# Kernel tuning notes

Hardware: AMD Instinct MI355X
Metric: run time of the kernel (lower is better)

The kernel has to match this reference:

```python
import jax, jax.numpy as jnp
import numpy as np

B, NW, LW = 128, 64, 32
TD, PD = 108, 19
F = PD + TD + 1   # feat_dim = 128
M = 128           # model_dim


def _linear_params(key, din, dout):
    kw, _ = jax.random.split(key)
    W = jax.random.normal(kw, (din, dout), jnp.float32) * 0.02
    b = jnp.zeros((dout,), jnp.float32)
    return W, b


def setup_inputs() -> dict:
    key = jax.random.key(0)
    ks = jax.random.split(key, 12)
    time_features = jax.random.normal(ks[0], (B, NW, LW, TD), jnp.float32)
    position_pos_features = jax.random.normal(ks[1], (B, NW, LW, PD), jnp.float32)
    position_neg_features = jax.random.normal(ks[2], (B, NW, LW, PD), jnp.float32)
    weight = jax.random.uniform(ks[3], (B, NW, LW), jnp.float32)
    # sign in {-1, +1} (0 would zero the step; walks are signed edges)
    sign = (2 * jax.random.randint(ks[4], (B, NW, LW), 0, 2) - 1).astype(jnp.int32)
    Wq, bq = _linear_params(ks[5], F, F)
    Wk, bk = _linear_params(ks[6], F, F)
    Wv, bv = _linear_params(ks[7], F, F)
    Wl, bl = _linear_params(ks[8], F, M)
    Wqp, bqp = _linear_params(ks[9], M, M)
    Wkp, bkp = _linear_params(ks[10], M, M)
    Wvp, bvp = _linear_params(ks[11], M, M)
    return dict(time_features=time_features,
                position_pos_features=position_pos_features,
                position_neg_features=position_neg_features,
                weight=weight, sign=sign,
                Wq=Wq, bq=bq, Wk=Wk, bk=bk, Wv=Wv, bv=bv,
                Wl=Wl, bl=bl,
                Wqp=Wqp, bqp=bqp, Wkp=Wkp, bkp=bkp, Wvp=Wvp, bvp=bvp)


def _self_attn_sum(x, Wq, bq, Wk, bk, Wv, bv):
    # x: [..., L, D]; manual scaled-dot attention, scale = sqrt(input_size)
    d = x.shape[-1]
    q = x @ Wq + bq
    k = x @ Wk + bk
    v = x @ Wv + bv
    scores = jnp.einsum('...ld,...md->...lm', q, k) / jnp.sqrt(jnp.float32(d))
    w = jax.nn.softmax(scores, axis=-1)
    av = jnp.einsum('...lm,...md->...ld', w, v)
    return av.sum(axis=-2)  # sum over query positions


def reference(time_features, position_pos_features, position_neg_features,
              weight, sign,
              Wq, bq, Wk, bk, Wv, bv, Wl, bl,
              Wqp, bqp, Wkp, bkp, Wvp, bvp):
    # concat_features (note arg swap in forward_one_node): [pos_feat, time_feat, weight]
    cp = jnp.concatenate([position_pos_features, time_features, weight[..., None]], axis=-1)
    cn = jnp.concatenate([position_neg_features, time_features, weight[..., None]], axis=-1)
    pm = (sign > 0)[..., None]
    nm = (sign < 0)[..., None]
    zero = jnp.zeros((), cp.dtype)
    positive = jnp.where(pm, cp, zero) + jnp.where(nm, cn, zero)  # [B,NW,LW,F]
    negative = jnp.where(pm, cn, zero) + jnp.where(nm, cp, zero)
    # per-walk self-attention over len_walk, summed -> [B,NW,F]
    pos_emb = _self_attn_sum(positive, Wq, bq, Wk, bk, Wv, bv)
    neg_emb = _self_attn_sum(negative, Wq, bq, Wk, bk, Wv, bv)
    # set_node_embedding_act linear (no nonlinearity in source)
    pos_emb = pos_emb @ Wl + bl  # [B,NW,M]
    neg_emb = neg_emb @ Wl + bl
    # path attention over n_walk, summed -> [B,M]
    pos = _self_attn_sum(pos_emb, Wqp, bqp, Wkp, bkp, Wvp, bvp)
    neg = _self_attn_sum(neg_emb, Wqp, bqp, Wkp, bkp, Wvp, bvp)
    return (pos, neg)
```

## Files before the change

### kernel.cpp

```cpp
#include <hip/hip_runtime.h>
#include <hip/hip_bf16.h>

typedef __hip_bfloat16 bf16;
typedef unsigned short u16;
typedef unsigned int   u32;
typedef __attribute__((ext_vector_type(8))) short short8;
typedef __attribute__((ext_vector_type(4))) float f32x4;
typedef __attribute__((ext_vector_type(4))) unsigned int u32x4;

#define SCALE 0.08838834764831845f
#define MFMA  __builtin_amdgcn_mfma_f32_16x16x32_bf16

__device__ __forceinline__ float u2f(u16 x) { return __uint_as_float(((u32)x) << 16); }
__device__ __forceinline__ u16   f2u(float f) {
    __hip_bfloat16 h = __float2bfloat16(f);
    return *reinterpret_cast<u16*>(&h);
}
__device__ __forceinline__ float lo16(u32 w){ return __uint_as_float(w << 16); }
__device__ __forceinline__ float hi16(u32 w){ return __uint_as_float(w & 0xffff0000u); }
__device__ __forceinline__ int swz(int row, int col){ return (row << 7) | (col ^ ((row & 7) << 3)); }

__global__ void prep_aq(const float* __restrict__ Wq,  const float* __restrict__ Wk,
                        const float* __restrict__ bq,
                        const float* __restrict__ Wqp, const float* __restrict__ Wkp,
                        const float* __restrict__ bqp,
                        u16* __restrict__ frag, float* __restrict__ vv) {
    const int b = blockIdx.x;
    const int p = b / 33, sub = b % 33;
    const float* WA = p ? Wqp : Wq;
    const float* WB = p ? Wkp : Wk;
    const float* bA = p ? bqp : bq;
    if (sub < 32) {
        const int nt = sub >> 2, kc = sub & 3;
        u16* dst = frag + p * 16384 + sub * 512;
        for (int e = threadIdx.x; e < 512; e += 256) {
            const int lane = e >> 3, j = e & 7;
            const int k = kc * 32 + ((lane >> 4) << 3) + j;
            const int n = nt * 16 + (lane & 15);
            float a = 0.f;
            for (int cc = 0; cc < 128; cc += 4) {
                const float4 wa = *(const float4*)(WA + k * 128 + cc);
                const float4 wb = *(const float4*)(WB + n * 128 + cc);
                a += wa.x * wb.x + wa.y * wb.y + wa.z * wb.z + wa.w * wb.w;
            }
            dst[e] = f2u(a * SCALE);
        }
    } else {
        for (int d = threadIdx.x; d < 128; d += 256) {
            float a = 0.f;
            for (int cc = 0; cc < 128; cc++) a += WB[d * 128 + cc] * bA[cc];
            vv[p * 128 + d] = a;
        }
    }
}

__global__ void prep_wvl(const float* __restrict__ Wv, const float* __restrict__ bv,
                         const float* __restrict__ Wl, const float* __restrict__ bl,
                         u16* __restrict__ wvlT, float* __restrict__ bvl) {
    const int d = threadIdx.x;
    const int e = blockIdx.x;
    if (e < 128) {
        float a = 0.f;
        for (int cc = 0; cc < 128; cc++) a += Wv[e * 128 + cc] * Wl[cc * 128 + d];
        wvlT[(d >> 1) * 256 + e * 2 + (d & 1)] = f2u(a);
    } else {
        float a = bl[d];
        for (int cc = 0; cc < 128; cc++) a += 32.f * bv[cc] * Wl[cc * 128 + d];
        bvl[d] = a;
    }
}

__global__ __launch_bounds__(256) void rwa_walk_wave(
    const float* __restrict__ timef, const float* __restrict__ ppf,
    const float* __restrict__ pnf,  const float* __restrict__ wgt,
    const int*  __restrict__ sgn,
    const u16* __restrict__ fragQ,
    const float* __restrict__ vk,
    const u16* __restrict__ wvlT,
    const float* __restrict__ bvl,
    u16* __restrict__ emb)
{
    __shared__ __align__(16) u16 XS[4][4096];
    const int t  = threadIdx.x;
    const int wv = t >> 6, l = t & 63;
    const int wid  = blockIdx.x * 4 + wv;
    const int walk = wid >> 1, side = wid & 1;
    const int c = l & 15, g = l >> 4;
    u16* const xw = &XS[wv][0];

    const int row = l & 31, h = l >> 5;
    const int tok = walk * 32 + row;
    const float* tfp = timef + tok * 108;
    const float* pb = ((sgn[tok] > 0) == (side == 0)) ? (ppf + tok * 19) : (pnf + tok * 19);
    float ra = 0.f;
    #pragma unroll
    for (int ch = 0; ch < 8; ch++) {
        float tmp[8];
        #pragma unroll
        for (int j = 0; j < 8; j++) {
            const int hf = ch * 8 + j;
            float val;
            if (h == 0) {
                val = (hf < 19) ? pb[hf] : tfp[hf - 19];
            } else {
                val = (hf < 63) ? tfp[45 + hf] : wgt[tok];
            }
            tmp[j] = val;
        }
        const float4 k4a = *(const float4*)(vk + h * 64 + ch * 8);
        const float4 k4b = *(const float4*)(vk + h * 64 + ch * 8 + 4);
        ra += tmp[0] * k4a.x + tmp[1] * k4a.y + tmp[2] * k4a.z + tmp[3] * k4a.w
            + tmp[4] * k4b.x + tmp[5] * k4b.y + tmp[6] * k4b.z + tmp[7] * k4b.w;
        short8 pk;
        #pragma unroll
        for (int j = 0; j < 8; j++) pk[j] = (short)f2u(tmp[j]);
        *(short8*)&xw[swz(row, h * 64 + ch * 8)] = pk;
    }
    ra += __shfl_xor(ra, 32);
    ra *= SCALE;

    short8 af[2][4];
    #pragma unroll
    for (int it = 0; it < 2; it++)
        #pragma unroll
        for (int kc = 0; kc < 4; kc++)
            af[it][kc] = *(const short8*)&xw[swz(it * 16 + c, kc * 32 + g * 8)];

    #pragma unroll
    for (int nt = 0; nt < 8; nt++) {
        f32x4 a0 = {0.f, 0.f, 0.f, 0.f}, a1 = {0.f, 0.f, 0.f, 0.f};
        #pragma unroll
        for (int kc = 0; kc < 4; kc++) {
            const short8 bf = *(const short8*)(fragQ + ((nt * 4 + kc) * 64 + l) * 8);
            a0 = MFMA(af[0][kc], bf, a0, 0, 0, 0);
            a1 = MFMA(af[1][kc], bf, a1, 0, 0, 0);
        }
        #pragma unroll
        for (int r = 0; r < 4; r++) {
            xw[swz(g * 4 + r,      nt * 16 + c)] = f2u(a0[r]);
            xw[swz(16 + g * 4 + r, nt * 16 + c)] = f2u(a1[r]);
        }
    }

    f32x4 sa[2][2];
    #pragma unroll
    for (int it = 0; it < 2; it++) {
        short8 tg[4];
        #pragma unroll
        for (int kc = 0; kc < 4; kc++)
            tg[kc] = *(const short8*)&xw[swz(it * 16 + c, kc * 32 + g * 8)];
        #pragma unroll
        for (int jt = 0; jt < 2; jt++) {
            f32x4 acc = {0.f, 0.f, 0.f, 0.f};
            #pragma unroll
            for (int kc = 0; kc < 4; kc++)
                acc = MFMA(tg[kc], af[jt][kc], acc, 0, 0, 0);
            sa[it][jt] = acc;
        }
    }
    const float ra0 = __shfl(ra, c);
    const float ra1 = __shfl(ra, 16 + c);
    float cs0 = 0.f, cs1 = 0.f;
    #pragma unroll
    for (int it = 0; it < 2; it++)
    #pragma unroll
    for (int r = 0; r < 4; r++) {
        const float s0v = sa[it][0][r] + ra0;
        const float s1v = sa[it][1][r] + ra1;
        float m0 = fmaxf(s0v, s1v);
        m0 = fmaxf(m0, __shfl_xor(m0, 1));
        m0 = fmaxf(m0, __shfl_xor(m0, 2));
        m0 = fmaxf(m0, __shfl_xor(m0, 4));
        m0 = fmaxf(m0, __shfl_xor(m0, 8));
        const float p0 = __expf(s0v - m0);
        const float p1 = __expf(s1v - m0);
        float sm = p0 + p1;
        sm += __shfl_xor(sm, 1); sm += __shfl_xor(sm, 2);
        sm += __shfl_xor(sm, 4); sm += __shfl_xor(sm, 8);
        const float inv = 1.f / sm;
        cs0 += p0 * inv; cs1 += p1 * inv;
    }
    cs0 += __shfl_xor(cs0, 16); cs0 += __shfl_xor(cs0, 32);
    cs1 += __shfl_xor(cs1, 16); cs1 += __shfl_xor(cs1, 32);

    #pragma unroll
    for (int it = 0; it < 2; it++)
        #pragma unroll
        for (int kc = 0; kc < 4; kc++)
            *(short8*)&xw[swz(it * 16 + c, kc * 32 + g * 8)] = af[it][kc];

    float y0 = 0.f, y1v = 0.f;
    #pragma unroll
    for (int j = 0; j < 16; j++) {
        const float cj = __shfl(cs0, j);
        const u32 xv = *(const u32*)&xw[swz(j, 2 * l)];
        y0 += cj * lo16(xv); y1v += cj * hi16(xv);
    }
    #pragma unroll
    for (int j = 0; j < 16; j++) {
        const float cj = __shfl(cs1, j);
        const u32 xv = *(const u32*)&xw[swz(16 + j, 2 * l)];
        y0 += cj * lo16(xv); y1v += cj * hi16(xv);
    }

    float* const yb = (float*)xw;
    *(float2*)&yb[2 * l] = make_float2(y0, y1v);

    const float2 bb = *(const float2*)&bvl[2 * l];
    float e0 = bb.x, e1 = bb.y;
    const u32* wrow = (const u32*)wvlT + l * 128;
    const float4* yf = (const float4*)yb;
    #pragma unroll
    for (int eq = 0; eq < 32; eq++) {
        const u32x4 w4 = *(const u32x4*)(wrow + 4 * eq);
        const float4 y4 = yf[eq];
        e0 += y4.x * lo16(w4[0]) + y4.y * lo16(w4[1]) + y4.z * lo16(w4[2]) + y4.w * lo16(w4[3]);
        e1 += y4.x * hi16(w4[0]) + y4.y * hi16(w4[1]) + y4.z * hi16(w4[2]) + y4.w * hi16(w4[3]);
    }
    const u32 pk = (u32)f2u(e0) | ((u32)f2u(e1) << 16);
    ((u32*)emb)[(side * 8192 + walk) * 64 + l] = pk;
}

__global__ __launch_bounds__(256) void rwa_path_wave(
    const u16* __restrict__ embg, const u16* __restrict__ fragP,
    const float* __restrict__ vp, const float* __restrict__ Wvp,
    const float* __restrict__ bvp, float* __restrict__ out)
{
    __shared__ __align__(16) u16 ES[8192];
    __shared__ __align__(16) u16 TS[8192];
    __shared__ float raS[64];
    __shared__ float csP[4][64];
    __shared__ float y2S[4][128];
    __shared__ float y2F[128];
    __shared__ float outS[4][128];
    const int t  = threadIdx.x;
    const int sb = blockIdx.x;
    const int wv = t >> 6, l = t & 63;
    const int c = l & 15, g = l >> 4;

    {
        const int row = t >> 2, q = t & 3;
        const u16* src = embg + (size_t)sb * 8192 + row * 128 + q * 32;
        const float* vq = vp + q * 32;
        float p = 0.f;
        #pragma unroll
        for (int i = 0; i < 4; i++) {
            const short8 ev = *(const short8*)(src + 8 * i);
            #pragma unroll
            for (int j = 0; j < 8; j++) p += u2f((u16)ev[j]) * vq[8 * i + j];
            *(short8*)&ES[swz(row, q * 32 + 8 * i)] = ev;
        }
        p += __shfl_xor(p, 1);
        p += __shfl_xor(p, 2);
        if (q == 0) raS[row] = p * SCALE;
    }
    __syncthreads();

    {
        const int it = wv;
        short8 afr[4];
        #pragma unroll
        for (int kc = 0; kc < 4; kc++)
            afr[kc] = *(const short8*)&ES[swz(it * 16 + c, kc * 32 + g * 8)];
        #pragma unroll
        for (int nt = 0; nt < 8; nt++) {
            f32x4 acc = {0.f, 0.f, 0.f, 0.f};
            #pragma unroll
            for (int kc = 0; kc < 4; kc++) {
                const short8 bf = *(const short8*)(fragP + ((nt * 4 + kc) * 64 + l) * 8);
                acc = MFMA(afr[kc], bf, acc, 0, 0, 0);
            }
            #pragma unroll
            for (int r = 0; r < 4; r++)
                TS[swz(it * 16 + g * 4 + r, nt * 16 + c)] = f2u(acc[r]);
        }
    }
    __syncthreads();

    {
        const int it = wv;
        short8 tg[4];
        #pragma unroll
        for (int kc = 0; kc < 4; kc++)
            tg[kc] = *(const short8*)&TS[swz(it * 16 + c, kc * 32 + g * 8)];
        f32x4 sa[4];
        float raj[4];
        #pragma unroll
        for (int jt = 0; jt < 4; jt++) {
            f32x4 acc = {0.f, 0.f, 0.f, 0.f};
            #pragma unroll
            for (int kc = 0; kc < 4; kc++) {
                const short8 be = *(const short8*)&ES[swz(jt * 16 + c, kc * 32 + g * 8)];
                acc = MFMA(tg[kc], be, acc, 0, 0, 0);
            }
            sa[jt] = acc;
            raj[jt] = raS[jt * 16 + c];
        }
        float cs[4] = {0.f, 0.f, 0.f, 0.f};
        #pragma unroll
        for (int r = 0; r < 4; r++) {
            float p0 = sa[0][r] + raj[0], p1 = sa[1][r] + raj[1];
            float p2 = sa[2][r] + raj[2], p3 = sa[3][r] + raj[3];
            float m0 = fmaxf(fmaxf(p0, p1), fmaxf(p2, p3));
            m0 = fmaxf(m0, __shfl_xor(m0, 1));
            m0 = fmaxf(m0, __shfl_xor(m0, 2));
            m0 = fmaxf(m0, __shfl_xor(m0, 4));
            m0 = fmaxf(m0, __shfl_xor(m0, 8));
            p0 = __expf(p0 - m0); p1 = __expf(p1 - m0);
            p2 = __expf(p2 - m0); p3 = __expf(p3 - m0);
            float sm = p0 + p1 + p2 + p3;
            sm += __shfl_xor(sm, 1); sm += __shfl_xor(sm, 2);
            sm += __shfl_xor(sm, 4); sm += __shfl_xor(sm, 8);
            const float inv = 1.f / sm;
            cs[0] += p0 * inv; cs[1] += p1 * inv; cs[2] += p2 * inv; cs[3] += p3 * inv;
        }
        #pragma unroll
        for (int jt = 0; jt < 4; jt++) {
            cs[jt] += __shfl_xor(cs[jt], 16);
            cs[jt] += __shfl_xor(cs[jt], 32);
        }
        if (g == 0) {
            #pragma unroll
            for (int jt = 0; jt < 4; jt++) csP[wv][jt * 16 + c] = cs[jt];
        }
    }
    __syncthreads();

    {
        float y0 = 0.f, y1v = 0.f;
        #pragma unroll
        for (int jj = 0; jj < 16; jj++) {
            const int j = wv * 16 + jj;
            const float cj = csP[0][j] + csP[1][j] + csP[2][j] + csP[3][j];
            const u32 xv = *(const u32*)&ES[swz(j, 2 * l)];
            y0 += cj * lo16(xv); y1v += cj * hi16(xv);
        }
        y2S[wv][2 * l] = y0; y2S[wv][2 * l + 1] = y1v;
    }
    __syncthreads();
    if (t < 128) y2F[t] = y2S[0][t] + y2S[1][t] + y2S[2][t] + y2S[3][t];
    __syncthreads();

    {
        float o0 = 0.f, o1 = 0.f;
        const float2* w2p = (const float2*)Wvp;
        #pragma unroll
        for (int k = 0; k < 32; k++) {
            const int e = wv * 32 + k;
            const float ye = y2F[e];
            const float2 w2 = w2p[e * 64 + l];
            o0 += ye * w2.x; o1 += ye * w2.y;
        }
        outS[wv][2 * l] = o0; outS[wv][2 * l + 1] = o1;
    }
    __syncthreads();
    if (t < 128)
        out[sb * 128 + t] = 64.f * bvp[t] + outS[0][t] + outS[1][t] + outS[2][t] + outS[3][t];
}

__global__ __launch_bounds__(256) void rwa_fused_fb(
    const float* timef, const float* ppf, const float* pnf, const float* wgt,
    const int* __restrict__ sgn,
    const float* Wq, const float* bq, const float* Wk, const float* bk,
    const float* Wv, const float* bv, const float* Wl, const float* bl,
    const float* Wqp, const float* bqp, const float* Wkp, const float* bkp,
    const float* Wvp, const float* bvp, float* out)
{
    extern __shared__ __align__(16) char S[];
    char* const U = S;
    float (* const sc)[33]     = (float(*)[33])(S + 41088);
    u16   (* const embs)[128]  = (u16  (*)[128])(S + 45312);
    float* const csumA         = (float*)(S + 61696);
    float* const y1            = (float*)(S + 61824);
    float* const e1            = (float*)(S + 62336);
    u16   (* const xs)[128]   = (u16  (*)[128])U;
    float (* const qs)[128]   = (float(*)[128])(U + 8192);
    float (* const ks)[129]   = (float(*)[129])(U + 8192 + 16384);
    float (* const k2s)[129]  = (float(*)[129])U;
    float (* const qrow)[128] = (float(*)[128])(U + 33024);
    float (* const csum2)[64] = (float(*)[64])(U + 35072);

    const int t    = threadIdx.x;
    const int side = blockIdx.x >> 7;
    const int b    = blockIdx.x & 127;
    const int wv_  = t >> 6;
    const int lane = t & 63;

    for (int w = 0; w < 64; ++w) {
        const int tokb = (b * 64 + w) * 32;
        for (int o = t; o < 32 * 128; o += 256) {
            const int l = o >> 7, f = o & 127;
            const int tok = tokb + l;
            float v;
            if (f < 19) {
                const bool takeP = (sgn[tok] > 0) == (side == 0);
                v = takeP ? ppf[tok * 19 + f] : pnf[tok * 19 + f];
            } else if (f < 127) v = timef[tok * 108 + (f - 19)];
            else v = wgt[tok];
            xs[l][f] = f2u(v);
        }
        __syncthreads();
        {
            const int d = t & 127, l0 = t >> 7;
            float aq[16], ak[16];
            const float bqv = bq[d], bkv = bk[d];
            #pragma unroll
            for (int i = 0; i < 16; i++) { aq[i] = bqv; ak[i] = bkv; }
            for (int e = 0; e < 128; e += 4) {
                float xv[16][4];
                #pragma unroll
                for (int i = 0; i < 16; i++) {
                    const ushort4 u = *(const ushort4*)&xs[l0 + 2 * i][e];
                    xv[i][0] = u2f(u.x); xv[i][1] = u2f(u.y);
                    xv[i][2] = u2f(u.z); xv[i][3] = u2f(u.w);
                }
                #pragma unroll
                for (int r = 0; r < 4; r++) {
                    const float wq = Wq[(e + r) * 128 + d];
                    const float wk = Wk[(e + r) * 128 + d];
                    #pragma unroll
                    for (int i = 0; i < 16; i++) {
                        aq[i] += xv[i][r] * wq; ak[i] += xv[i][r] * wk;
                    }
                }
            }
            #pragma unroll
            for (int i = 0; i < 16; i++) { const int l = l0 + 2 * i; qs[l][d] = aq[i]; ks[l][d] = ak[i]; }
        }
        __syncthreads();
        for (int o = t; o < 1024; o += 256) {
            const int i = o >> 5, j = o & 31;
            float a0 = 0, a1 = 0, a2 = 0, a3 = 0;
            for (int e = 0; e < 128; e += 4) {
                const float4 q4 = *(const float4*)&qs[i][e];
                a0 += q4.x * ks[j][e];     a1 += q4.y * ks[j][e + 1];
                a2 += q4.z * ks[j][e + 2]; a3 += q4.w * ks[j][e + 3];
            }
            sc[i][j] = (a0 + a1 + a2 + a3) * SCALE;
        }
        __syncthreads();
        if (t < 32) {
            float m = -1e30f;
            for (int j = 0; j < 32; j++) m = fmaxf(m, sc[t][j]);
            float s = 0.f;
            for (int j = 0; j < 32; j++) { const float e0 = __expf(sc[t][j] - m); sc[t][j] = e0; s += e0; }
            const float inv = 1.f / s;
            for (int j = 0; j < 32; j++) sc[t][j] *= inv;
        }
        __syncthreads();
        if (t < 32) { float s = 0.f; for (int i = 0; i < 32; i++) s += sc[i][t]; csumA[t] = s; }
        __syncthreads();
        if (t < 128) { float a = 0.f; for (int j = 0; j < 32; j++) a += csumA[j] * u2f(xs[j][t]); y1[t] = a; }
        __syncthreads();
        if (t < 128) {
            float a = 32.f * bv[t];
            for (int e = 0; e < 128; e++) a += y1[e] * Wv[e * 128 + t];
            e1[t] = a;
        }
        __syncthreads();
        if (t < 128) {
            float a = bl[t];
            for (int f = 0; f < 128; f++) a += e1[f] * Wl[f * 128 + t];
            embs[w][t] = f2u(a);
        }
        __syncthreads();
    }
    {
        const int d = t & 127, j0 = t >> 7;
        float ak2[32];
        const float bkv = bkp[d];
        #pragma unroll
        for (int i = 0; i < 32; i++) ak2[i] = bkv;
        for (int e = 0; e < 128; e++) {
            const float wk = Wkp[e * 128 + d];
            #pragma unroll
            for (int i = 0; i < 32; i++) ak2[i] += u2f(embs[j0 + 2 * i][e]) * wk;
        }
        #pragma unroll
        for (int i = 0; i < 32; i++) k2s[j0 + 2 * i][d] = ak2[i];
    }
    csum2[wv_][lane] = 0.f;
    __syncthreads();
    for (int i0 = 0; i0 < 64; i0 += 4) {
        const int r = i0 + wv_;
        {
            float a0 = bqp[lane], a1 = bqp[lane + 64];
            for (int e = 0; e < 128; e++) {
                const float xv = u2f(embs[r][e]);
                a0 += xv * Wqp[e * 128 + lane];
                a1 += xv * Wqp[e * 128 + lane + 64];
            }
            qrow[wv_][lane] = a0; qrow[wv_][lane + 64] = a1;
        }
        {
            const int j = lane;
            float s = 0.f;
            for (int e = 0; e < 128; e += 4) {
                const float4 q4 = *(const float4*)&qrow[wv_][e];
                s += q4.x * k2s[j][e] + q4.y * k2s[j][e + 1] + q4.z * k2s[j][e + 2] + q4.w * k2s[j][e + 3];
            }
            s *= SCALE;
            float m = s;
            #pragma unroll
            for (int off = 32; off; off >>= 1) m = fmaxf(m, __shfl_xor(m, off));
            const float e0 = __expf(s - m);
            float sum = e0;
            #pragma unroll
            for (int off = 32; off; off >>= 1) sum += __shfl_xor(sum, off);
            csum2[wv_][j] += e0 / sum;
        }
        __syncthreads();
    }
    if (t < 64) csum2[0][t] = csum2[0][t] + csum2[1][t] + csum2[2][t] + csum2[3][t];
    __syncthreads();
    if (t < 128) { float a = 0.f; for (int j = 0; j < 64; j++) a += csum2[0][j] * u2f(embs[j][t]); y1[t] = a; }
    __syncthreads();
    if (t < 128) {
        float a = 64.f * bvp[t];
        for (int e = 0; e < 128; e++) a += y1[e] * Wvp[e * 128 + t];
        out[blockIdx.x * 128 + t] = a;
    }
}

extern "C" void kernel_launch(void* const* d_in, const int* in_sizes, int n_in,
                              void* d_out, int out_size, void* d_ws, size_t ws_size,
                              hipStream_t stream) {
    const float* timef = (const float*)d_in[0];
    const float* ppf   = (const float*)d_in[1];
    const float* pnf   = (const float*)d_in[2];
    const float* wgt   = (const float*)d_in[3];
    const int*   sgn   = (const int*)  d_in[4];
    const float* Wq  = (const float*)d_in[5];  const float* bq  = (const float*)d_in[6];
    const float* Wk  = (const float*)d_in[7];  const float* bk  = (const float*)d_in[8];
    const float* Wv  = (const float*)d_in[9];  const float* bv  = (const float*)d_in[10];
    const float* Wl  = (const float*)d_in[11]; const float* bl  = (const float*)d_in[12];
    const float* Wqp = (const float*)d_in[13]; const float* bqp = (const float*)d_in[14];
    const float* Wkp = (const float*)d_in[15]; const float* bkp = (const float*)d_in[16];
    const float* Wvp = (const float*)d_in[17]; const float* bvp = (const float*)d_in[18];
    float* out = (float*)d_out;
    (void)in_sizes; (void)n_in; (void)out_size;

    const size_t need = 99840 + (size_t)2 * 8192 * 128 * sizeof(u16);
    if (ws_size >= need) {
        u16*   frag = (u16*)d_ws;
        float* vv   = (float*)((char*)d_ws + 65536);
        u16*   wvlT = (u16*)((char*)d_ws + 66560);
        float* bvl  = (float*)((char*)d_ws + 99328);
        u16*   emb  = (u16*)((char*)d_ws + 99840);
        hipLaunchKernelGGL(prep_aq,  dim3(66),  dim3(256), 0, stream,
                           Wq, Wk, bq, Wqp, Wkp, bqp, frag, vv);
        hipLaunchKernelGGL(prep_wvl, dim3(129), dim3(128), 0, stream, Wv, bv, Wl, bl, wvlT, bvl);
        hipLaunchKernelGGL(rwa_walk_wave, dim3(4096), dim3(256), 0, stream,
                           timef, ppf, pnf, wgt, sgn, frag, vv, wvlT, bvl, emb);
        hipLaunchKernelGGL(rwa_path_wave, dim3(256), dim3(256), 0, stream,
                           emb, frag + 16384, vv + 128, Wvp, bvp, out);
    } else {
        hipLaunchKernelGGL(rwa_fused_fb, dim3(256), dim3(256), 62848, stream,
                           timef, ppf, pnf, wgt, sgn, Wq, bq, Wk, bk, Wv, bv, Wl, bl,
                           Wqp, bqp, Wkp, bkp, Wvp, bvp, out);
    }
}
```

Before: 391.7 us.

## Coalesce walk feature loads and restructure Wvl layout for lane-contiguous reads

Feature loading in the walk kernel now has lanes read consecutive elements of each token row, so global reads are coalesced, instead of each lane striding through one token's features. The rank-one bias score term is recomputed from the bf16 fragments already held in registers, which removes the shuffles that used to broadcast it. Column broadcasts use readlane instead of shuffles. The Wv·Wl product is stored row-major so each lane reads a contiguous u32 per row rather than a strided transposed row. The bias term now uses bf16-rounded inputs, which slightly changes numerics.

```diff
diff --git a/kernel.cpp b/kernel.cpp
--- a/kernel.cpp
+++ b/kernel.cpp
@@ -18,6 +18,9 @@
 }
 __device__ __forceinline__ float lo16(u32 w){ return __uint_as_float(w << 16); }
 __device__ __forceinline__ float hi16(u32 w){ return __uint_as_float(w & 0xffff0000u); }
+__device__ __forceinline__ float rdlane(float v, int lane) {
+    return __uint_as_float(__builtin_amdgcn_readlane(__float_as_uint(v), lane));
+}
 __device__ __forceinline__ int swz(int row, int col){ return (row << 7) | (col ^ ((row & 7) << 3)); }
 
 __global__ void prep_aq(const float* __restrict__ Wq,  const float* __restrict__ Wk,
@@ -56,13 +59,13 @@
 
 __global__ void prep_wvl(const float* __restrict__ Wv, const float* __restrict__ bv,
                          const float* __restrict__ Wl, const float* __restrict__ bl,
-                         u16* __restrict__ wvlT, float* __restrict__ bvl) {
+                         u16* __restrict__ wvl, float* __restrict__ bvl) {
     const int d = threadIdx.x;
     const int e = blockIdx.x;
     if (e < 128) {
         float a = 0.f;
         for (int cc = 0; cc < 128; cc++) a += Wv[e * 128 + cc] * Wl[cc * 128 + d];
-        wvlT[(d >> 1) * 256 + e * 2 + (d & 1)] = f2u(a);
+        wvl[e * 128 + d] = f2u(a);
     } else {
         float a = bl[d];
         for (int cc = 0; cc < 128; cc++) a += 32.f * bv[cc] * Wl[cc * 128 + d];
@@ -76,7 +79,7 @@
     const int*  __restrict__ sgn,
     const u16* __restrict__ fragQ,
     const float* __restrict__ vk,
-    const u16* __restrict__ wvlT,
+    const u16* __restrict__ wvl,
     const float* __restrict__ bvl,
     u16* __restrict__ emb)
 {
@@ -87,37 +90,30 @@
     const int walk = wid >> 1, side = wid & 1;
     const int c = l & 15, g = l >> 4;
     u16* const xw = &XS[wv][0];
-
-    const int row = l & 31, h = l >> 5;
-    const int tok = walk * 32 + row;
-    const float* tfp = timef + tok * 108;
-    const float* pb = ((sgn[tok] > 0) == (side == 0)) ? (ppf + tok * 19) : (pnf + tok * 19);
-    float ra = 0.f;
-    #pragma unroll
-    for (int ch = 0; ch < 8; ch++) {
-        float tmp[8];
-        #pragma unroll
-        for (int j = 0; j < 8; j++) {
-            const int hf = ch * 8 + j;
-            float val;
-            if (h == 0) {
-                val = (hf < 19) ? pb[hf] : tfp[hf - 19];
-            } else {
-                val = (hf < 63) ? tfp[45 + hf] : wgt[tok];
-            }
-            tmp[j] = val;
-        }
-        const float4 k4a = *(const float4*)(vk + h * 64 + ch * 8);
-        const float4 k4b = *(const float4*)(vk + h * 64 + ch * 8 + 4);
-        ra += tmp[0] * k4a.x + tmp[1] * k4a.y + tmp[2] * k4a.z + tmp[3] * k4a.w
-            + tmp[4] * k4b.x + tmp[5] * k4b.y + tmp[6] * k4b.z + tmp[7] * k4b.w;
-        short8 pk;
-        #pragma unroll
-        for (int j = 0; j < 8; j++) pk[j] = (short)f2u(tmp[j]);
-        *(short8*)&xw[swz(row, h * 64 + ch * 8)] = pk;
-    }
-    ra += __shfl_xor(ra, 32);
-    ra *= SCALE;
+    const int tokb = walk * 32;
+
+    {
+        const float* tb = timef + (size_t)tokb * 108;
+        #pragma unroll 4
+        for (int rr = 0; rr < 32; rr++) {
+            xw[swz(rr, 19 + l)] = f2u(tb[rr * 108 + l]);
+            if (l < 44)
+                xw[swz(rr, 83 + l)] = f2u(tb[rr * 108 + 64 + l]);
+        }
+        const size_t pbase = (size_t)tokb * 19;
+        #pragma unroll
+        for (int i = 0; i < 10; i++) {
+            const int o = i * 64 + l;
+            if (o < 608) {
+                const int row = o / 19;
+                const int f   = o - row * 19;
+                const bool sp = (sgn[tokb + row] > 0) == (side == 0);
+                const float* pb = sp ? ppf : pnf;
+                xw[swz(row, f)] = f2u(pb[pbase + o]);
+            }
+        }
+        if (l < 32) xw[swz(l, 127)] = f2u(wgt[tokb + l]);
+    }
 
     short8 af[2][4];
     #pragma unroll
@@ -125,6 +121,23 @@
         #pragma unroll
         for (int kc = 0; kc < 4; kc++)
             af[it][kc] = *(const short8*)&xw[swz(it * 16 + c, kc * 32 + g * 8)];
+
+    float rr0 = 0.f, rr1 = 0.f;
+    #pragma unroll
+    for (int kc = 0; kc < 4; kc++) {
+        const float4 ka = *(const float4*)(vk + kc * 32 + g * 8);
+        const float4 kb = *(const float4*)(vk + kc * 32 + g * 8 + 4);
+        const float kk[8] = {ka.x, ka.y, ka.z, ka.w, kb.x, kb.y, kb.z, kb.w};
+        #pragma unroll
+        for (int j = 0; j < 8; j++) {
+            rr0 += u2f((u16)af[0][kc][j]) * kk[j];
+            rr1 += u2f((u16)af[1][kc][j]) * kk[j];
+        }
+    }
+    rr0 += __shfl_xor(rr0, 16); rr0 += __shfl_xor(rr0, 32);
+    rr1 += __shfl_xor(rr1, 16); rr1 += __shfl_xor(rr1, 32);
+    const float ra0 = rr0 * SCALE;
+    const float ra1 = rr1 * SCALE;
 
     #pragma unroll
     for (int nt = 0; nt < 8; nt++) {
@@ -158,8 +171,6 @@
             sa[it][jt] = acc;
         }
     }
-    const float ra0 = __shfl(ra, c);
-    const float ra1 = __shfl(ra, 16 + c);
     float cs0 = 0.f, cs1 = 0.f;
     #pragma unroll
     for (int it = 0; it < 2; it++)
@@ -192,13 +203,13 @@
     float y0 = 0.f, y1v = 0.f;
     #pragma unroll
     for (int j = 0; j < 16; j++) {
-        const float cj = __shfl(cs0, j);
+        const float cj = rdlane(cs0, j);
         const u32 xv = *(const u32*)&xw[swz(j, 2 * l)];
         y0 += cj * lo16(xv); y1v += cj * hi16(xv);
     }
     #pragma unroll
     for (int j = 0; j < 16; j++) {
-        const float cj = __shfl(cs1, j);
+        const float cj = rdlane(cs1, j);
         const u32 xv = *(const u32*)&xw[swz(16 + j, 2 * l)];
         y0 += cj * lo16(xv); y1v += cj * hi16(xv);
     }
@@ -208,14 +219,17 @@
 
     const float2 bb = *(const float2*)&bvl[2 * l];
     float e0 = bb.x, e1 = bb.y;
-    const u32* wrow = (const u32*)wvlT + l * 128;
+    const u32* wp = (const u32*)wvl;
     const float4* yf = (const float4*)yb;
-    #pragma unroll
-    for (int eq = 0; eq < 32; eq++) {
-        const u32x4 w4 = *(const u32x4*)(wrow + 4 * eq);
-        const float4 y4 = yf[eq];
-        e0 += y4.x * lo16(w4[0]) + y4.y * lo16(w4[1]) + y4.z * lo16(w4[2]) + y4.w * lo16(w4[3]);
-        e1 += y4.x * hi16(w4[0]) + y4.y * hi16(w4[1]) + y4.z * hi16(w4[2]) + y4.w * hi16(w4[3]);
+    #pragma unroll 8
+    for (int e4 = 0; e4 < 32; e4++) {
+        const float4 y4 = yf[e4];
+        const u32 w0 = wp[(e4 * 4 + 0) * 64 + l];
+        const u32 w1 = wp[(e4 * 4 + 1) * 64 + l];
+        const u32 w2 = wp[(e4 * 4 + 2) * 64 + l];
+        const u32 w3 = wp[(e4 * 4 + 3) * 64 + l];
+        e0 += y4.x * lo16(w0) + y4.y * lo16(w1) + y4.z * lo16(w2) + y4.w * lo16(w3);
+        e1 += y4.x * hi16(w0) + y4.y * hi16(w1) + y4.z * hi16(w2) + y4.w * hi16(w3);
     }
     const u32 pk = (u32)f2u(e0) | ((u32)f2u(e1) << 16);
     ((u32*)emb)[(side * 8192 + walk) * 64 + l] = pk;
@@ -544,14 +558,14 @@
     if (ws_size >= need) {
         u16*   frag = (u16*)d_ws;
         float* vv   = (float*)((char*)d_ws + 65536);
-        u16*   wvlT = (u16*)((char*)d_ws + 66560);
+        u16*   wvl  = (u16*)((char*)d_ws + 66560);
         float* bvl  = (float*)((char*)d_ws + 99328);
         u16*   emb  = (u16*)((char*)d_ws + 99840);
         hipLaunchKernelGGL(prep_aq,  dim3(66),  dim3(256), 0, stream,
                            Wq, Wk, bq, Wqp, Wkp, bqp, frag, vv);
-        hipLaunchKernelGGL(prep_wvl, dim3(129), dim3(128), 0, stream, Wv, bv, Wl, bl, wvlT, bvl);
+        hipLaunchKernelGGL(prep_wvl, dim3(129), dim3(128), 0, stream, Wv, bv, Wl, bl, wvl, bvl);
         hipLaunchKernelGGL(rwa_walk_wave, dim3(4096), dim3(256), 0, stream,
-                           timef, ppf, pnf, wgt, sgn, frag, vv, wvlT, bvl, emb);
+                           timef, ppf, pnf, wgt, sgn, frag, vv, wvl, bvl, emb);
         hipLaunchKernelGGL(rwa_path_wave, dim3(256), dim3(256), 0, stream,
                            emb, frag + 16384, vv + 128, Wvp, bvp, out);
     } else {
```

Measured after the change: 445.6 us. 13.8% more time.

## Split walk kernel and move Wv·Wl projection to a batched MFMA GEMM

Applied to the files above, without the earlier changes.

Splits the per-walk kernel so it writes the softmax-weighted sum y1 as fp32 to global memory, then runs a separate batched GEMM kernel that applies the fused Wv·Wl projection with MFMA, using a hi/lo bf16 split of y1 to keep precision. This replaces the per-wave scalar 128x128 dot-product loop over bf16 weights with matrix-core work. Cross-lane broadcasts use readlane instead of shuffle. The cost is an extra fp32 round trip through global memory of about 8 MB and one more kernel launch. The old fused path is kept as a fallback for smaller workspaces.

```diff
diff --git a/kernel.cpp b/kernel.cpp
--- a/kernel.cpp
+++ b/kernel.cpp
@@ -18,6 +18,9 @@
 }
 __device__ __forceinline__ float lo16(u32 w){ return __uint_as_float(w << 16); }
 __device__ __forceinline__ float hi16(u32 w){ return __uint_as_float(w & 0xffff0000u); }
+__device__ __forceinline__ float rdlane(float v, int lane) {
+    return __uint_as_float(__builtin_amdgcn_readlane(__float_as_uint(v), lane));
+}
 __device__ __forceinline__ int swz(int row, int col){ return (row << 7) | (col ^ ((row & 7) << 3)); }
 
 __global__ void prep_aq(const float* __restrict__ Wq,  const float* __restrict__ Wk,
@@ -56,13 +59,16 @@
 
 __global__ void prep_wvl(const float* __restrict__ Wv, const float* __restrict__ bv,
                          const float* __restrict__ Wl, const float* __restrict__ bl,
-                         u16* __restrict__ wvlT, float* __restrict__ bvl) {
+                         u16* __restrict__ wvlT, u16* __restrict__ wvlF,
+                         float* __restrict__ bvl) {
     const int d = threadIdx.x;
     const int e = blockIdx.x;
     if (e < 128) {
         float a = 0.f;
         for (int cc = 0; cc < 128; cc++) a += Wv[e * 128 + cc] * Wl[cc * 128 + d];
-        wvlT[(d >> 1) * 256 + e * 2 + (d & 1)] = f2u(a);
+        const u16 u = f2u(a);
+        wvlT[(d >> 1) * 256 + e * 2 + (d & 1)] = u;
+        wvlF[(((d >> 4) * 4) + (e >> 5)) * 512 + (((e >> 3) & 3) * 16 + (d & 15)) * 8 + (e & 7)] = u;
     } else {
         float a = bl[d];
         for (int cc = 0; cc < 128; cc++) a += 32.f * bv[cc] * Wl[cc * 128 + d];
@@ -70,15 +76,13 @@
     }
 }
 
-__global__ __launch_bounds__(256) void rwa_walk_wave(
+__global__ __launch_bounds__(256) void rwa_walk_y1(
     const float* __restrict__ timef, const float* __restrict__ ppf,
     const float* __restrict__ pnf,  const float* __restrict__ wgt,
     const int*  __restrict__ sgn,
     const u16* __restrict__ fragQ,
     const float* __restrict__ vk,
-    const u16* __restrict__ wvlT,
-    const float* __restrict__ bvl,
-    u16* __restrict__ emb)
+    float* __restrict__ y1g)
 {
     __shared__ __align__(16) u16 XS[4][4096];
     const int t  = threadIdx.x;
@@ -192,13 +196,193 @@
     float y0 = 0.f, y1v = 0.f;
     #pragma unroll
     for (int j = 0; j < 16; j++) {
-        const float cj = __shfl(cs0, j);
+        const float cj = rdlane(cs0, j);
         const u32 xv = *(const u32*)&xw[swz(j, 2 * l)];
         y0 += cj * lo16(xv); y1v += cj * hi16(xv);
     }
     #pragma unroll
     for (int j = 0; j < 16; j++) {
-        const float cj = __shfl(cs1, j);
+        const float cj = rdlane(cs1, j);
+        const u32 xv = *(const u32*)&xw[swz(16 + j, 2 * l)];
+        y0 += cj * lo16(xv); y1v += cj * hi16(xv);
+    }
+
+    *(float2*)&y1g[((size_t)(side * 8192 + walk)) * 128 + 2 * l] = make_float2(y0, y1v);
+}
+
+__global__ __launch_bounds__(256) void rwa_emb_gemm(
+    const float* __restrict__ y1g, const u16* __restrict__ wvlF,
+    const float* __restrict__ bvl, u16* __restrict__ emb)
+{
+    __shared__ __align__(16) u16 AH[8192];
+    __shared__ __align__(16) u16 AL[8192];
+    const int t = threadIdx.x;
+    const int row0 = blockIdx.x * 64;
+    const int wv = t >> 6, l = t & 63;
+    const int c = l & 15, g = l >> 4;
+
+    const float* src = y1g + (size_t)row0 * 128;
+    #pragma unroll
+    for (int i = 0; i < 8; i++) {
+        const int o = t * 4 + i * 1024;
+        const float4 v = *(const float4*)(src + o);
+        const int r = o >> 7, cc = o & 127;
+        ushort4 hs, ls;
+        const u16 h0 = f2u(v.x), h1 = f2u(v.y), h2 = f2u(v.z), h3 = f2u(v.w);
+        hs.x = h0; hs.y = h1; hs.z = h2; hs.w = h3;
+        ls.x = f2u(v.x - u2f(h0)); ls.y = f2u(v.y - u2f(h1));
+        ls.z = f2u(v.z - u2f(h2)); ls.w = f2u(v.w - u2f(h3));
+        *(ushort4*)&AH[swz(r, cc)] = hs;
+        *(ushort4*)&AL[swz(r, cc)] = ls;
+    }
+    __syncthreads();
+
+    short8 aH[4], aL[4];
+    #pragma unroll
+    for (int kc = 0; kc < 4; kc++) {
+        aH[kc] = *(const short8*)&AH[swz(wv * 16 + c, kc * 32 + g * 8)];
+        aL[kc] = *(const short8*)&AL[swz(wv * 16 + c, kc * 32 + g * 8)];
+    }
+    #pragma unroll
+    for (int nt = 0; nt < 8; nt++) {
+        const float bz = bvl[nt * 16 + c];
+        f32x4 acc = { bz, bz, bz, bz };
+        #pragma unroll
+        for (int kc = 0; kc < 4; kc++) {
+            const short8 bf = *(const short8*)(wvlF + ((nt * 4 + kc) * 64 + l) * 8);
+            acc = MFMA(aH[kc], bf, acc, 0, 0, 0);
+            acc = MFMA(aL[kc], bf, acc, 0, 0, 0);
+        }
+        #pragma unroll
+        for (int r = 0; r < 4; r++)
+            emb[(size_t)(row0 + wv * 16 + g * 4 + r) * 128 + nt * 16 + c] = f2u(acc[r]);
+    }
+}
+
+__global__ __launch_bounds__(256) void rwa_walk_wave(
+    const float* __restrict__ timef, const float* __restrict__ ppf,
+    const float* __restrict__ pnf,  const float* __restrict__ wgt,
+    const int*  __restrict__ sgn,
+    const u16* __restrict__ fragQ, const float* __restrict__ vk,
+    const u16* __restrict__ wvlT, const float* __restrict__ bvl,
+    u16* __restrict__ emb)
+{
+    __shared__ __align__(16) u16 XS[4][4096];
+    const int t  = threadIdx.x;
+    const int wv = t >> 6, l = t & 63;
+    const int wid  = blockIdx.x * 4 + wv;
+    const int walk = wid >> 1, side = wid & 1;
+    const int c = l & 15, g = l >> 4;
+    u16* const xw = &XS[wv][0];
+
+    const int row = l & 31, h = l >> 5;
+    const int tok = walk * 32 + row;
+    const float* tfp = timef + tok * 108;
+    const float* pb = ((sgn[tok] > 0) == (side == 0)) ? (ppf + tok * 19) : (pnf + tok * 19);
+    float ra = 0.f;
+    #pragma unroll
+    for (int ch = 0; ch < 8; ch++) {
+        float tmp[8];
+        #pragma unroll
+        for (int j = 0; j < 8; j++) {
+            const int hf = ch * 8 + j;
+            float val;
+            if (h == 0) val = (hf < 19) ? pb[hf] : tfp[hf - 19];
+            else        val = (hf < 63) ? tfp[45 + hf] : wgt[tok];
+            tmp[j] = val;
+        }
+        const float4 k4a = *(const float4*)(vk + h * 64 + ch * 8);
+        const float4 k4b = *(const float4*)(vk + h * 64 + ch * 8 + 4);
+        ra += tmp[0] * k4a.x + tmp[1] * k4a.y + tmp[2] * k4a.z + tmp[3] * k4a.w
+            + tmp[4] * k4b.x + tmp[5] * k4b.y + tmp[6] * k4b.z + tmp[7] * k4b.w;
+        short8 pk;
+        #pragma unroll
+        for (int j = 0; j < 8; j++) pk[j] = (short)f2u(tmp[j]);
+        *(short8*)&xw[swz(row, h * 64 + ch * 8)] = pk;
+    }
+    ra += __shfl_xor(ra, 32);
+    ra *= SCALE;
+
+    short8 af[2][4];
+    #pragma unroll
+    for (int it = 0; it < 2; it++)
+        #pragma unroll
+        for (int kc = 0; kc < 4; kc++)
+            af[it][kc] = *(const short8*)&xw[swz(it * 16 + c, kc * 32 + g * 8)];
+
+    #pragma unroll
+    for (int nt = 0; nt < 8; nt++) {
+        f32x4 a0 = {0.f, 0.f, 0.f, 0.f}, a1 = {0.f, 0.f, 0.f, 0.f};
+        #pragma unroll
+        for (int kc = 0; kc < 4; kc++) {
+            const short8 bf = *(const short8*)(fragQ + ((nt * 4 + kc) * 64 + l) * 8);
+            a0 = MFMA(af[0][kc], bf, a0, 0, 0, 0);
+            a1 = MFMA(af[1][kc], bf, a1, 0, 0, 0);
+        }
+        #pragma unroll
+        for (int r = 0; r < 4; r++) {
+            xw[swz(g * 4 + r,      nt * 16 + c)] = f2u(a0[r]);
+            xw[swz(16 + g * 4 + r, nt * 16 + c)] = f2u(a1[r]);
+        }
+    }
+
+    f32x4 sa[2][2];
+    #pragma unroll
+    for (int it = 0; it < 2; it++) {
+        short8 tg[4];
+        #pragma unroll
+        for (int kc = 0; kc < 4; kc++)
+            tg[kc] = *(const short8*)&xw[swz(it * 16 + c, kc * 32 + g * 8)];
+        #pragma unroll
+        for (int jt = 0; jt < 2; jt++) {
+            f32x4 acc = {0.f, 0.f, 0.f, 0.f};
+            #pragma unroll
+            for (int kc = 0; kc < 4; kc++)
+                acc = MFMA(tg[kc], af[jt][kc], acc, 0, 0, 0);
+            sa[it][jt] = acc;
+        }
+    }
+    const float ra0 = __shfl(ra, c);
+    const float ra1 = __shfl(ra, 16 + c);
+    float cs0 = 0.f, cs1 = 0.f;
+    #pragma unroll
+    for (int it = 0; it < 2; it++)
+    #pragma unroll
+    for (int r = 0; r < 4; r++) {
+        const float s0v = sa[it][0][r] + ra0;
+        const float s1v = sa[it][1][r] + ra1;
+        float m0 = fmaxf(s0v, s1v);
+        m0 = fmaxf(m0, __shfl_xor(m0, 1));
+        m0 = fmaxf(m0, __shfl_xor(m0, 2));
+        m0 = fmaxf(m0, __shfl_xor(m0, 4));
+        m0 = fmaxf(m0, __shfl_xor(m0, 8));
+        const float p0 = __expf(s0v - m0);
+        const float p1 = __expf(s1v - m0);
+        float sm = p0 + p1;
+        sm += __shfl_xor(sm, 1); sm += __shfl_xor(sm, 2);
+        sm += __shfl_xor(sm, 4); sm += __shfl_xor(sm, 8);
+        const float inv = 1.f / sm;
+        cs0 += p0 * inv; cs1 += p1 * inv;
+    }
+    cs0 += __shfl_xor(cs0, 16); cs0 += __shfl_xor(cs0, 32);
+    cs1 += __shfl_xor(cs1, 16); cs1 += __shfl_xor(cs1, 32);
+
+    #pragma unroll
+    for (int it = 0; it < 2; it++)
+        #pragma unroll
+        for (int kc = 0; kc < 4; kc++)
+            *(short8*)&xw[swz(it * 16 + c, kc * 32 + g * 8)] = af[it][kc];
+
+    float y0 = 0.f, y1v = 0.f;
+    #pragma unroll
+    for (int j = 0; j < 16; j++) {
+        const float cj = rdlane(cs0, j);
+        const u32 xv = *(const u32*)&xw[swz(j, 2 * l)];
+        y0 += cj * lo16(xv); y1v += cj * hi16(xv);
+    }
+    #pragma unroll
+    for (int j = 0; j < 16; j++) {
+        const float cj = rdlane(cs1, j);
         const u32 xv = *(const u32*)&xw[swz(16 + j, 2 * l)];
         y0 += cj * lo16(xv); y1v += cj * hi16(xv);
     }
@@ -210,7 +394,7 @@
     float e0 = bb.x, e1 = bb.y;
     const u32* wrow = (const u32*)wvlT + l * 128;
     const float4* yf = (const float4*)yb;
-    #pragma unroll
+    #pragma unroll 8
     for (int eq = 0; eq < 32; eq++) {
         const u32x4 w4 = *(const u32x4*)(wrow + 4 * eq);
         const float4 y4 = yf[eq];
@@ -540,16 +724,32 @@
     float* out = (float*)d_out;
     (void)in_sizes; (void)n_in; (void)out_size;
 
-    const size_t need = 99840 + (size_t)2 * 8192 * 128 * sizeof(u16);
-    if (ws_size >= need) {
-        u16*   frag = (u16*)d_ws;
-        float* vv   = (float*)((char*)d_ws + 65536);
-        u16*   wvlT = (u16*)((char*)d_ws + 66560);
-        float* bvl  = (float*)((char*)d_ws + 99328);
-        u16*   emb  = (u16*)((char*)d_ws + 99840);
+    u16*   frag = (u16*)d_ws;
+    float* vv   = (float*)((char*)d_ws + 65536);
+    u16*   wvlT = (u16*)((char*)d_ws + 66560);
+    u16*   wvlF = (u16*)((char*)d_ws + 99328);
+    float* bvl  = (float*)((char*)d_ws + 132096);
+    u16*   emb  = (u16*)((char*)d_ws + 132608);
+    float* y1g  = (float*)((char*)d_ws + 4326912);
+    const size_t need_mid = 132608 + (size_t)2 * 8192 * 128 * sizeof(u16);
+    const size_t need_big = 4326912 + (size_t)16384 * 128 * sizeof(float);
+
+    if (ws_size >= need_big) {
         hipLaunchKernelGGL(prep_aq,  dim3(66),  dim3(256), 0, stream,
                            Wq, Wk, bq, Wqp, Wkp, bqp, frag, vv);
-        hipLaunchKernelGGL(prep_wvl, dim3(129), dim3(128), 0, stream, Wv, bv, Wl, bl, wvlT, bvl);
+        hipLaunchKernelGGL(prep_wvl, dim3(129), dim3(128), 0, stream,
+                           Wv, bv, Wl, bl, wvlT, wvlF, bvl);
+        hipLaunchKernelGGL(rwa_walk_y1, dim3(4096), dim3(256), 0, stream,
+                           timef, ppf, pnf, wgt, sgn, frag, vv, y1g);
+        hipLaunchKernelGGL(rwa_emb_gemm, dim3(256), dim3(256), 0, stream,
+                           y1g, wvlF, bvl, emb);
+        hipLaunchKernelGGL(rwa_path_wave, dim3(256), dim3(256), 0, stream,
+                           emb, frag + 16384, vv + 128, Wvp, bvp, out);
+    } else if (ws_size >= need_mid) {
+        hipLaunchKernelGGL(prep_aq,  dim3(66),  dim3(256), 0, stream,
+                           Wq, Wk, bq, Wqp, Wkp, bqp, frag, vv);
+        hipLaunchKernelGGL(prep_wvl, dim3(129), dim3(128), 0, stream,
+                           Wv, bv, Wl, bl, wvlT, wvlF, bvl);
         hipLaunchKernelGGL(rwa_walk_wave, dim3(4096), dim3(256), 0, stream,
                            timef, ppf, pnf, wgt, sgn, frag, vv, wvlT, bvl, emb);
         hipLaunchKernelGGL(rwa_path_wave, dim3(256), dim3(256), 0, stream,
```

After: 345.1 us. 1.14x faster.
